# Kernel tuning notes

Measured on AMD Instinct MI355X. Metric: run time of the kernel, lower is better.

Reference implementation:

```python
import jax, jax.numpy as jnp
import numpy as np

DIM = 128
HEADS = 8
DH = DIM // HEADS
WIN = (4, 4, 4)
TOPK = 4
EPS = 1e-6


def _ln(x, g, b):
    mu = jnp.mean(x, -1, keepdims=True)
    var = jnp.mean((x - mu) ** 2, -1, keepdims=True)
    return (x - mu) * jax.lax.rsqrt(var + EPS) * g + b


def _win3d(x, p1, p2, p3):
    # x: [B,S,H,W,C] -> [B, p1*p2*p3, Ms, Mh, Mw, C]
    B, S, H, W, C = x.shape
    Ms, Mh, Mw = S // p1, H // p2, W // p3
    x = x.reshape(B, p1, Ms, p2, Mh, p3, Mw, C)
    x = x.transpose(0, 1, 3, 5, 2, 4, 6, 7)
    return x.reshape(B, p1 * p2 * p3, Ms, Mh, Mw, C)


def setup_inputs() -> dict:
    key = jax.random.key(0)
    ks = jax.random.split(key, 20)

    def lin(k, din, dout):
        return jax.random.normal(k, (din, dout), jnp.float32) * 0.02

    return {
        "x_in": jax.random.normal(ks[0], (2, 128, 16, 32, 32), jnp.float32),
        "x_g_in": jax.random.normal(ks[1], (2, 128, 8, 16, 16), jnp.float32),
        # Atten (global branch)
        "qkv_w": lin(ks[2], DIM, 3 * DIM), "qkv_b": jnp.zeros((3 * DIM,), jnp.float32),
        "proj_w": lin(ks[3], DIM, DIM), "proj_b": jnp.zeros((DIM,), jnp.float32),
        # shared LayerNorm (self.norm1 is reused everywhere in the original)
        "ln_g": jnp.ones((DIM,), jnp.float32), "ln_b": jnp.zeros((DIM,), jnp.float32),
        # mlp (global branch FFN)
        "mlp_w1": lin(ks[4], DIM, 4 * DIM), "mlp_b1": jnp.zeros((4 * DIM,), jnp.float32),
        "mlp_w2": lin(ks[5], 4 * DIM, DIM), "mlp_b2": jnp.zeros((DIM,), jnp.float32),
        # TopkRouting
        "rq_w": lin(ks[6], DIM, DIM), "rq_b": jnp.zeros((DIM,), jnp.float32),
        "rk_w": lin(ks[7], DIM, DIM), "rk_b": jnp.zeros((DIM,), jnp.float32),
        # fused qkv over concatenated local+gathered-global tokens
        "gqkv_w": lin(ks[8], DIM, 3 * DIM), "gqkv_b": jnp.zeros((3 * DIM,), jnp.float32),
        "wo_w": lin(ks[9], DIM, DIM), "wo_b": jnp.zeros((DIM,), jnp.float32),
        # mlp2 (local branch FFN)
        "mlp2_w1": lin(ks[10], DIM, 4 * DIM), "mlp2_b1": jnp.zeros((4 * DIM,), jnp.float32),
        "mlp2_w2": lin(ks[11], 4 * DIM, DIM), "mlp2_b2": jnp.zeros((DIM,), jnp.float32),
    }


def reference(x_in, x_g_in, qkv_w, qkv_b, proj_w, proj_b, ln_g, ln_b,
              mlp_w1, mlp_b1, mlp_w2, mlp_b2, rq_w, rq_b, rk_w, rk_b,
              gqkv_w, gqkv_b, wo_w, wo_b, mlp2_w1, mlp2_b1, mlp2_w2, mlp2_b2):
    B, C, S, H, W = x_in.shape
    Ms, Mh, Mw = WIN
    p1, p2, p3 = S // Ms, H // Mh, W // Mw  # pads are zero for these shapes
    nw, w3l = p1 * p2 * p3, Ms * Mh * Mw
    scale = DIM ** -0.5  # BiLevelRoutingAttention.scale = dim**-0.5 (not per-head)

    x = jnp.transpose(x_in, (0, 2, 3, 4, 1))  # [B,S,H,W,C]
    shortcut_l = _win3d(x, p1, p2, p3).reshape(B, nw, w3l, C)

    # ---- global branch: full self-attention + FFN ----
    _, _, gS, gH, gW = x_g_in.shape
    gN = gS * gH * gW
    xg = jnp.transpose(x_g_in, (0, 2, 3, 4, 1)).reshape(B, gN, C)
    h = _ln(xg, ln_g, ln_b)
    qkv = (h @ qkv_w + qkv_b).reshape(B, gN, 3, HEADS, DH).transpose(2, 0, 3, 1, 4)
    q, k, v = qkv[0], qkv[1], qkv[2]
    a = jax.nn.softmax(jnp.einsum('bhnd,bhmd->bhnm', q, k) * DH ** -0.5, axis=-1)
    o = jnp.einsum('bhnm,bhmd->bhnd', a, v).transpose(0, 2, 1, 3).reshape(B, gN, C)
    xg = (o @ proj_w + proj_b) + xg
    xg4 = xg.reshape(B, gS, gH, gW, C)
    h = _ln(xg4, ln_g, ln_b)
    xg4 = xg4 + (jax.nn.gelu(h @ mlp_w1 + mlp_b1, approximate=False) @ mlp_w2 + mlp_b2)

    # ---- top-k window routing ----
    swg = _win3d(xg4, p1, p2, p3)  # [B,nw,gMs,gMh,gMw,C]
    w3g = swg.shape[2] * swg.shape[3] * swg.shape[4]
    g_win = swg.mean((2, 3, 4))  # [B,nw,C]
    qh = g_win @ rq_w + rq_b
    kh = g_win @ rk_w + rk_b
    logit = jnp.einsum('bnc,bmc->bnm', qh * scale, kh)
    _tvals, tidx = jax.lax.top_k(logit, TOPK)  # r_weight is computed but unused in the original forward

    # gather top-k global windows' tokens per local window
    gflat = swg.reshape(B, nw, w3g, C)
    gath = jax.vmap(lambda kv, idx: kv[idx])(gflat, tidx)  # [B,nw,topk,w3g,C]
    sc = jnp.concatenate([shortcut_l, gath.reshape(B, nw, TOPK * w3g, C)], axis=2)
    w3 = w3l + TOPK * w3g

    # ---- local+routed attention over concatenated tokens ----
    qkvp = _ln(sc, ln_g, ln_b) @ gqkv_w + gqkv_b
    qp, kp, vp = jnp.split(qkvp, 3, axis=-1)
    qp = qp.reshape(B, nw, w3, HEADS, DH)
    kp = kp.reshape(B, nw, w3, HEADS, DH)
    vp = vp.reshape(B, nw, w3, HEADS, DH)
    aw = jax.nn.softmax(jnp.einsum('bnqhd,bnkhd->bnhqk', qp * scale, kp), axis=-1)
    out = jnp.einsum('bnhqk,bnkhd->bnqhd', aw, vp).reshape(B, nw, w3, C)

    l = out[:, :, :w3l] @ wo_w + wo_b + shortcut_l
    l = l.reshape(B, p1, p2, p3, Ms, Mh, Mw, C).transpose(0, 1, 4, 2, 5, 3, 6, 7).reshape(B, S, H, W, C)
    l = l + (jax.nn.gelu(_ln(l, ln_g, ln_b) @ mlp2_w1 + mlp2_b1, approximate=False) @ mlp2_w2 + mlp2_b2)

    l_out = jnp.transpose(l, (0, 4, 1, 2, 3))
    g_out = jnp.transpose(xg4, (0, 4, 1, 2, 3))
    return (l_out, g_out)
```

## Files before the change

### kernel.cpp

```cpp
#include <hip/hip_runtime.h>
#include <hip/hip_bf16.h>
#include <math.h>

#define BATCH 2
#define CDIM 128
#define SS 16
#define HH_ 32
#define WW_ 32
#define NSP (SS*HH_*WW_)
#define GS 8
#define GH 16
#define GW 16
#define GN (GS*GH*GW)
#define HEADS 8
#define DH 16
#define NW 256
#define W3L 64
#define W3G 8
#define TOPK 4
#define W3 (W3L + TOPK*W3G)
#define LN_EPS 1e-6f
#define ROUTE_SCALE 0.08838834764831845f
#define GATTN_SCALE 0.25f

typedef short bshort8 __attribute__((ext_vector_type(8)));
typedef float f32x4 __attribute__((ext_vector_type(4)));

__device__ __forceinline__ unsigned short f2bf(float f) {
    unsigned int u = __float_as_uint(f);
    unsigned int r = (u + 0x7fffu + ((u >> 16) & 1u)) >> 16;
    return (unsigned short)r;
}
__device__ __forceinline__ float gelu_exact(float x) {
    return 0.5f * x * (1.0f + erff(x * 0.70710678118654752f));
}
__device__ __forceinline__ float shfl_sum32(float v) {
#pragma unroll
    for (int m = 16; m > 0; m >>= 1) v += __shfl_xor(v, m);
    return v;
}
__device__ __forceinline__ float shfl_sum16(float v) {
#pragma unroll
    for (int m = 8; m > 0; m >>= 1) v += __shfl_xor(v, m);
    return v;
}
__device__ __forceinline__ float shfl_sum8(float v) {
#pragma unroll
    for (int m = 4; m > 0; m >>= 1) v += __shfl_xor(v, m);
    return v;
}

__global__ __launch_bounds__(256) void k_wprep_all(const float* __restrict__ gqkv_w,
        const float* __restrict__ m2_w1, const float* __restrict__ m2_w2,
        const float* __restrict__ proj_w, const float* __restrict__ mlp_w1,
        const float* __restrict__ mlp_w2, const float* __restrict__ wo_w,
        const float* __restrict__ qkv_w,
        unsigned short* __restrict__ wt, unsigned short* __restrict__ w1t,
        unsigned short* __restrict__ w2t, unsigned short* __restrict__ projt,
        unsigned short* __restrict__ gw1t, unsigned short* __restrict__ gw2t,
        unsigned short* __restrict__ wot, unsigned short* __restrict__ qkvt) {
    int id = blockIdx.x * 256 + threadIdx.x;
    if (id < 49152) {
        int n = id >> 7, k = id & 127;
        float v = gqkv_w[k * 384 + n];
        if (n < 128) v *= ROUTE_SCALE;
        wt[id] = f2bf(v);
    } else if (id < 114688) {
        int i = id - 49152; int n = i >> 7, k = i & 127;
        w1t[i] = f2bf(m2_w1[k * 512 + n]);
    } else if (id < 180224) {
        int i = id - 114688; int n = i >> 9, k = i & 511;
        w2t[i] = f2bf(m2_w2[k * 128 + n]);
    } else if (id < 196608) {
        int i = id - 180224; int n = i >> 7, k = i & 127;
        projt[i] = f2bf(proj_w[k * 128 + n]);
    } else if (id < 262144) {
        int i = id - 196608; int n = i >> 7, k = i & 127;
        gw1t[i] = f2bf(mlp_w1[k * 512 + n]);
    } else if (id < 327680) {
        int i = id - 262144; int n = i >> 9, k = i & 511;
        gw2t[i] = f2bf(mlp_w2[k * 128 + n]);
    } else if (id < 344064) {
        int i = id - 327680; int n = i >> 7, k = i & 127;
        wot[i] = f2bf(wo_w[k * 128 + n]);
    } else {
        int i = id - 344064; int n = i >> 7, k = i & 127;
        float v = qkv_w[k * 384 + n];
        if (n < 128) v *= GATTN_SCALE;
        qkvt[i] = f2bf(v);
    }
}

__global__ __launch_bounds__(256) void k_gqkv_mfma(const float* __restrict__ xg_in,
        const unsigned short* __restrict__ qkvt, const float* __restrict__ qkv_b,
        const float* __restrict__ ln_g, const float* __restrict__ ln_b,
        float* __restrict__ xg, unsigned short* __restrict__ qgb,
        unsigned short* __restrict__ kgb, unsigned short* __restrict__ vgtb) {
    int blk = blockIdx.x; int b = blk >> 7; int n0 = (blk & 127) * 16;
    int t = threadIdx.x; int w = t >> 6; int lane = t & 63;
    int l15 = lane & 15, quad = lane >> 4;
    __shared__ __align__(16) float xs[16 * 132];
    __shared__ __align__(16) unsigned short h[16 * 136];
    f32x4 zero4 = {0.f, 0.f, 0.f, 0.f};

    {
        int c = t >> 1, j0 = (t & 1) * 8;
        const float* src = xg_in + ((size_t)(b * 128 + c)) * GN + n0 + j0;
        float4 v0 = *(const float4*)src;
        float4 v1 = *(const float4*)(src + 4);
        xs[(j0 + 0) * 132 + c] = v0.x; xs[(j0 + 1) * 132 + c] = v0.y;
        xs[(j0 + 2) * 132 + c] = v0.z; xs[(j0 + 3) * 132 + c] = v0.w;
        xs[(j0 + 4) * 132 + c] = v1.x; xs[(j0 + 5) * 132 + c] = v1.y;
        xs[(j0 + 6) * 132 + c] = v1.z; xs[(j0 + 7) * 132 + c] = v1.w;
    }
    __syncthreads();
    {
        int j = t >> 4, p = t & 15, c0 = p * 8;
        float vv[8]; float s1 = 0.f;
#pragma unroll
        for (int i = 0; i < 8; i++) { vv[i] = xs[j * 132 + c0 + i]; s1 += vv[i]; }
        s1 = shfl_sum16(s1);
        float mu = s1 * (1.0f / 128.0f);
        float s2 = 0.f;
#pragma unroll
        for (int i = 0; i < 8; i++) { float d = vv[i] - mu; s2 += d * d; }
        s2 = shfl_sum16(s2);
        float rs = rsqrtf(s2 * (1.0f / 128.0f) + LN_EPS);
        float* dst = xg + ((size_t)(b * GN) + n0 + j) * 128 + c0;
        *(float4*)dst = *(float4*)&vv[0];
        *(float4*)(dst + 4) = *(float4*)&vv[4];
        unsigned short hb[8];
#pragma unroll
        for (int i4 = 0; i4 < 2; i4++) {
            float4 g4 = *(const float4*)(ln_g + c0 + i4 * 4);
            float4 b4 = *(const float4*)(ln_b + c0 + i4 * 4);
            hb[i4 * 4 + 0] = f2bf((vv[i4 * 4 + 0] - mu) * rs * g4.x + b4.x);
            hb[i4 * 4 + 1] = f2bf((vv[i4 * 4 + 1] - mu) * rs * g4.y + b4.y);
            hb[i4 * 4 + 2] = f2bf((vv[i4 * 4 + 2] - mu) * rs * g4.z + b4.z);
            hb[i4 * 4 + 3] = f2bf((vv[i4 * 4 + 3] - mu) * rs * g4.w + b4.w);
        }
        *(ushort4*)&h[j * 136 + c0] = *(ushort4*)&hb[0];
        *(ushort4*)&h[j * 136 + c0 + 4] = *(ushort4*)&hb[4];
    }
    __syncthreads();

    bshort8 a[4];
#pragma unroll
    for (int ks = 0; ks < 4; ks++)
        a[ks] = *(const bshort8*)(h + l15 * 136 + ks * 32 + quad * 8);
    int bh_base = b * HEADS;
#pragma unroll
    for (int part = 0; part < 2; part++) {
#pragma unroll
        for (int which = 0; which < 2; which++) {
            int nt = 2 * w + which;
            int ncol = part * 128 + nt * 16;
            f32x4 acc = zero4;
#pragma unroll
            for (int ks = 0; ks < 4; ks++) {
                bshort8 bfr = *(const bshort8*)(qkvt + (size_t)(ncol + l15) * 128 + ks * 32 + quad * 8);
                acc = __builtin_amdgcn_mfma_f32_16x16x32_bf16(a[ks], bfr, acc, 0, 0, 0);
            }
            float bias = qkv_b[ncol + l15] * (part == 0 ? GATTN_SCALE : 1.f);
            unsigned short* dst = (part == 0) ? qgb : kgb;
#pragma unroll
            for (int r = 0; r < 4; r++)
                dst[((size_t)(bh_base + nt) * GN + n0 + quad * 4 + r) * DH + l15] = f2bf(acc[r] + bias);
        }
    }
#pragma unroll
    for (int which = 0; which < 2; which++) {
        int mtv = 2 * w + which;
        f32x4 acc = zero4;
#pragma unroll
        for (int ks = 0; ks < 4; ks++) {
            bshort8 aw = *(const bshort8*)(qkvt + (size_t)(256 + mtv * 16 + l15) * 128 + ks * 32 + quad * 8);
            acc = __builtin_amdgcn_mfma_f32_16x16x32_bf16(aw, a[ks], acc, 0, 0, 0);
        }
#pragma unroll
        for (int r = 0; r < 4; r++) {
            float bias = qkv_b[256 + mtv * 16 + quad * 4 + r];
            vgtb[((size_t)(bh_base + mtv) * DH + quad * 4 + r) * GN + n0 + l15] = f2bf(acc[r] + bias);
        }
    }
}

__global__ __launch_bounds__(256) void k_gattn_mfma(const unsigned short* __restrict__ qgb,
        const unsigned short* __restrict__ kgb, const unsigned short* __restrict__ vgtb,
        float* __restrict__ og) {
    int blk = blockIdx.x;
    int bh = blk >> 7; int qt = (blk & 127) << 4;
    int b = bh >> 3, hh = bh & 7;
    int t = threadIdx.x; int w = t >> 6; int lane = t & 63;
    int col = lane & 15, quad = lane >> 4;
    __shared__ __align__(16) unsigned short Pbuf[4 * 16 * 40];
    __shared__ float po[4][64][4];
    __shared__ float pl[4][64][4];

    bshort8 aq = {0, 0, 0, 0, 0, 0, 0, 0};
    if (quad < 2)
        aq = *(const bshort8*)(qgb + ((size_t)bh * GN + qt + col) * DH + quad * 8);

    f32x4 o = {0.f, 0.f, 0.f, 0.f};
    float lsum[4] = {0.f, 0.f, 0.f, 0.f};
    const unsigned short* kb = kgb + (size_t)bh * GN * DH;
    const unsigned short* vb = vgtb + (size_t)bh * DH * GN;
    unsigned short* pb = Pbuf + w * (16 * 40);
    int row0 = quad * 4;
    int kbeg = w * 512;
    for (int kc = kbeg; kc < kbeg + 512; kc += 32) {
        bshort8 bk0 = {0, 0, 0, 0, 0, 0, 0, 0};
        bshort8 bk1 = {0, 0, 0, 0, 0, 0, 0, 0};
        if (quad < 2) {
            bk0 = *(const bshort8*)(kb + (size_t)(kc + col) * DH + quad * 8);
            bk1 = *(const bshort8*)(kb + (size_t)(kc + 16 + col) * DH + quad * 8);
        }
        f32x4 z = {0.f, 0.f, 0.f, 0.f};
        f32x4 s0 = __builtin_amdgcn_mfma_f32_16x16x32_bf16(aq, bk0, z, 0, 0, 0);
        f32x4 s1 = __builtin_amdgcn_mfma_f32_16x16x32_bf16(aq, bk1, z, 0, 0, 0);
        float p0[4], p1[4];
#pragma unroll
        for (int r = 0; r < 4; r++) {
            p0[r] = __expf(s0[r]); p1[r] = __expf(s1[r]);
            lsum[r] += p0[r] + p1[r];
        }
#pragma unroll
        for (int r = 0; r < 4; r++) {
            pb[(row0 + r) * 40 + col] = f2bf(p0[r]);
            pb[(row0 + r) * 40 + 16 + col] = f2bf(p1[r]);
        }
        bshort8 pA = *(const bshort8*)(pb + col * 40 + quad * 8);
        bshort8 bv = *(const bshort8*)(vb + (size_t)col * GN + kc + quad * 8);
        o = __builtin_amdgcn_mfma_f32_16x16x32_bf16(pA, bv, o, 0, 0, 0);
    }
#pragma unroll
    for (int r = 0; r < 4; r++) {
        float v = lsum[r];
        v += __shfl_xor(v, 1); v += __shfl_xor(v, 2);
        v += __shfl_xor(v, 4); v += __shfl_xor(v, 8);
        lsum[r] = v;
    }
#pragma unroll
    for (int r = 0; r < 4; r++) { po[w][lane][r] = o[r]; pl[w][lane][r] = lsum[r]; }
    __syncthreads();
    if (w == 0) {
#pragma unroll
        for (int r = 0; r < 4; r++) {
            float os = po[0][lane][r] + po[1][lane][r] + po[2][lane][r] + po[3][lane][r];
            float ls = pl[0][lane][r] + pl[1][lane][r] + pl[2][lane][r] + pl[3][lane][r];
            og[((size_t)(b * GN) + qt + quad * 4 + r) * 128 + hh * 16 + col] = os / ls;
        }
    }
}

__global__ __launch_bounds__(256) void k_gmlp_mfma(const float* __restrict__ og,
        const float* __restrict__ xg,
        const unsigned short* __restrict__ projt, const float* __restrict__ proj_b,
        const float* __restrict__ ln_g, const float* __restrict__ ln_b,
        const unsigned short* __restrict__ gw1t, const float* __restrict__ b1,
        const unsigned short* __restrict__ gw2t, const float* __restrict__ b2,
        float* __restrict__ xg4, float* __restrict__ gout) {
    int blk = blockIdx.x; int b = blk >> 7; int n0g = (blk & 127) * 16;
    int t = threadIdx.x; int w = t >> 6; int lane = t & 63;
    int l15 = lane & 15, quad = lane >> 4;
    __shared__ __align__(16) unsigned short ao[16 * 136];
    __shared__ __align__(16) float xs[16 * 132];
    __shared__ __align__(16) unsigned short h[16 * 136];
    __shared__ __align__(16) unsigned short h1[16 * 520];
    float* of32 = (float*)h1;
    f32x4 zero4 = {0.f, 0.f, 0.f, 0.f};

    {
        int j = t >> 4, p = t & 15, c0 = p * 8;
        size_t base = ((size_t)(b * GN) + n0g + j) * 128 + c0;
        float4 v0 = *(const float4*)(og + base);
        float4 v1 = *(const float4*)(og + base + 4);
        ushort4 u0 = { f2bf(v0.x), f2bf(v0.y), f2bf(v0.z), f2bf(v0.w) };
        ushort4 u1 = { f2bf(v1.x), f2bf(v1.y), f2bf(v1.z), f2bf(v1.w) };
        *(ushort4*)&ao[j * 136 + c0] = u0;
        *(ushort4*)&ao[j * 136 + c0 + 4] = u1;
        *(float4*)&xs[j * 132 + c0] = *(const float4*)(xg + base);
        *(float4*)&xs[j * 132 + c0 + 4] = *(const float4*)(xg + base + 4);
    }
    __syncthreads();

    {
        bshort8 a[4];
#pragma unroll
        for (int ks = 0; ks < 4; ks++)
            a[ks] = *(const bshort8*)(ao + l15 * 136 + ks * 32 + quad * 8);
#pragma unroll
        for (int nt = 0; nt < 2; nt++) {
            int n0 = w * 32 + nt * 16;
            f32x4 acc = zero4;
#pragma unroll
            for (int ks = 0; ks < 4; ks++) {
                bshort8 bfr = *(const bshort8*)(projt + (n0 + l15) * 128 + ks * 32 + quad * 8);
                acc = __builtin_amdgcn_mfma_f32_16x16x32_bf16(a[ks], bfr, acc, 0, 0, 0);
            }
            float bias = proj_b[n0 + l15];
#pragma unroll
            for (int r = 0; r < 4; r++) {
                int m = quad * 4 + r;
                xs[m * 132 + n0 + l15] += acc[r] + bias;
            }
        }
    }
    __syncthreads();

    {
        int j = t >> 4, p = t & 15, c0 = p * 8;
        float vv[8]; float s1 = 0.f;
#pragma unroll
        for (int i = 0; i < 8; i++) { vv[i] = xs[j * 132 + c0 + i]; s1 += vv[i]; }
        s1 = shfl_sum16(s1);
        float mu = s1 * (1.0f / 128.0f);
        float s2 = 0.f;
#pragma unroll
        for (int i = 0; i < 8; i++) { float d = vv[i] - mu; s2 += d * d; }
        s2 = shfl_sum16(s2);
        float rs = rsqrtf(s2 * (1.0f / 128.0f) + LN_EPS);
        unsigned short hb[8];
#pragma unroll
        for (int i4 = 0; i4 < 2; i4++) {
            float4 g4 = *(const float4*)(ln_g + c0 + i4 * 4);
            float4 b4 = *(const float4*)(ln_b + c0 + i4 * 4);
            hb[i4 * 4 + 0] = f2bf((vv[i4 * 4 + 0] - mu) * rs * g4.x + b4.x);
            hb[i4 * 4 + 1] = f2bf((vv[i4 * 4 + 1] - mu) * rs * g4.y + b4.y);
            hb[i4 * 4 + 2] = f2bf((vv[i4 * 4 + 2] - mu) * rs * g4.z + b4.z);
            hb[i4 * 4 + 3] = f2bf((vv[i4 * 4 + 3] - mu) * rs * g4.w + b4.w);
        }
        *(ushort4*)&h[j * 136 + c0] = *(ushort4*)&hb[0];
        *(ushort4*)&h[j * 136 + c0 + 4] = *(ushort4*)&hb[4];
    }
    __syncthreads();

    {
        bshort8 a[4];
#pragma unroll
        for (int ks = 0; ks < 4; ks++)
            a[ks] = *(const bshort8*)(h + l15 * 136 + ks * 32 + quad * 8);
#pragma unroll
        for (int nt = 0; nt < 8; nt++) {
            int n0 = w * 128 + nt * 16;
            f32x4 acc = zero4;
#pragma unroll
            for (int ks = 0; ks < 4; ks++) {
                bshort8 bfr = *(const bshort8*)(gw1t + (size_t)(n0 + l15) * 128 + ks * 32 + quad * 8);
                acc = __builtin_amdgcn_mfma_f32_16x16x32_bf16(a[ks], bfr, acc, 0, 0, 0);
            }
            float bias = b1[n0 + l15];
#pragma unroll
            for (int r = 0; r < 4; r++)
                h1[(quad * 4 + r) * 520 + n0 + l15] = f2bf(gelu_exact(acc[r] + bias));
        }
    }
    __syncthreads();

    f32x4 acc2[2]; acc2[0] = zero4; acc2[1] = zero4;
#pragma unroll 4
    for (int ks = 0; ks < 16; ks++) {
        bshort8 a = *(const bshort8*)(h1 + l15 * 520 + ks * 32 + quad * 8);
#pragma unroll
        for (int nt = 0; nt < 2; nt++) {
            int n0 = w * 32 + nt * 16;
            bshort8 bfr = *(const bshort8*)(gw2t + (size_t)(n0 + l15) * 512 + ks * 32 + quad * 8);
            acc2[nt] = __builtin_amdgcn_mfma_f32_16x16x32_bf16(a, bfr, acc2[nt], 0, 0, 0);
        }
    }
    __syncthreads();

    {
#pragma unroll
        for (int nt = 0; nt < 2; nt++) {
            int n0 = w * 32 + nt * 16;
            float bias = b2[n0 + l15];
#pragma unroll
            for (int r = 0; r < 4; r++) {
                int m = quad * 4 + r;
                float ov = xs[m * 132 + n0 + l15] + acc2[nt][r] + bias;
                of32[m * 132 + n0 + l15] = ov;
                xg4[((size_t)(b * GN) + n0g + m) * 128 + n0 + l15] = ov;
            }
        }
    }
    __syncthreads();

    {
        int cw = t >> 1, hf = t & 1, j0 = hf * 8;
        float* dst = gout + ((size_t)(b * 128 + cw)) * GN + n0g + j0;
#pragma unroll
        for (int i4 = 0; i4 < 2; i4++) {
            float4 ov = { of32[(j0 + i4 * 4 + 0) * 132 + cw], of32[(j0 + i4 * 4 + 1) * 132 + cw],
                          of32[(j0 + i4 * 4 + 2) * 132 + cw], of32[(j0 + i4 * 4 + 3) * 132 + cw] };
            *(float4*)(dst + i4 * 4) = ov;
        }
    }
}

__global__ void k_routing_qk(const float* __restrict__ xg4,
                             const float* __restrict__ rq_w, const float* __restrict__ rq_b,
                             const float* __restrict__ rk_w, const float* __restrict__ rk_b,
                             float* __restrict__ qh, float* __restrict__ kh) {
    int wid = blockIdx.x; int b = wid / NW, n = wid % NW;
    int c = threadIdx.x;
    int i1 = n / 64, i2 = (n / 8) % 8, i3 = n % 8;
    __shared__ float g[CDIM];
    float s = 0.f;
#pragma unroll
    for (int j = 0; j < W3G; j++) {
        int ds = j >> 2, dh = (j >> 1) & 1, dw = j & 1;
        int gi = ((i1 * 2 + ds) * GH + (i2 * 2 + dh)) * GW + (i3 * 2 + dw);
        s += xg4[((size_t)(b * GN + gi)) * CDIM + c];
    }
    g[c] = s * (1.0f / W3G);
    __syncthreads();
    float aq = rq_b[c], ak = rk_b[c];
    for (int k = 0; k < CDIM; k++) { float gv = g[k]; aq = fmaf(gv, rq_w[k * CDIM + c], aq); ak = fmaf(gv, rk_w[k * CDIM + c], ak); }
    qh[(size_t)wid * CDIM + c] = aq;
    kh[(size_t)wid * CDIM + c] = ak;
}

__global__ void k_topk(const float* __restrict__ qh, const float* __restrict__ kh,
                       int* __restrict__ tidx) {
    int wid = blockIdx.x; int b = wid / NW;
    int m = threadIdx.x;
    __shared__ float q[CDIM];
    __shared__ float lv[NW];
    __shared__ int li[NW];
    if (m < CDIM) q[m] = qh[(size_t)wid * CDIM + m] * ROUTE_SCALE;
    __syncthreads();
    float acc = 0.f;
    const float* kr = kh + ((size_t)b * NW + m) * CDIM;
    for (int k = 0; k < CDIM; k++) acc = fmaf(q[k], kr[k], acc);
#pragma unroll
    for (int sel = 0; sel < TOPK; sel++) {
        lv[m] = acc; li[m] = m; __syncthreads();
#pragma unroll
        for (int s = 128; s > 0; s >>= 1) {
            if (m < s) {
                if (lv[m + s] > lv[m] || (lv[m + s] == lv[m] && li[m + s] < li[m])) {
                    lv[m] = lv[m + s]; li[m] = li[m + s];
                }
            }
            __syncthreads();
        }
        int best = li[0]; __syncthreads();
        if (m == best) acc = -1e30f;
        if (m == 0) tidx[wid * TOPK + sel] = best;
    }
}

__global__ __launch_bounds__(256) void k_lnsc_local(const float* __restrict__ x_in,
        const float* __restrict__ ln_g, const float* __restrict__ ln_b,
        unsigned short* __restrict__ lnsc) {
    int blk = blockIdx.x;
    int wt = blk & 1; int hh = (blk >> 1) & 31; int s = (blk >> 6) & 15; int b = blk >> 10;
    int w0 = wt * 16;
    int t = threadIdx.x;
    __shared__ float tile[16][132];
    {
        int c = t >> 1; int wq = (t & 1) * 8;
        const float* src = x_in + (((size_t)(b * 128 + c) * SS + s)) * 1024 + hh * 32 + w0 + wq;
        float4 v0 = *(const float4*)src;
        float4 v1 = *(const float4*)(src + 4);
        tile[wq + 0][c] = v0.x; tile[wq + 1][c] = v0.y; tile[wq + 2][c] = v0.z; tile[wq + 3][c] = v0.w;
        tile[wq + 4][c] = v1.x; tile[wq + 5][c] = v1.y; tile[wq + 6][c] = v1.z; tile[wq + 7][c] = v1.w;
    }
    __syncthreads();
    int w = t >> 4; int j = t & 15;
    float vals[8];
    float s1 = 0.f;
#pragma unroll
    for (int i = 0; i < 8; i++) { vals[i] = tile[w][j * 8 + i]; s1 += vals[i]; }
    s1 = shfl_sum16(s1);
    float mu = s1 * (1.0f / 128.0f);
    float s2 = 0.f;
#pragma unroll
    for (int i = 0; i < 8; i++) { float d = vals[i] - mu; s2 += d * d; }
    s2 = shfl_sum16(s2);
    float rs = rsqrtf(s2 * (1.0f / 128.0f) + LN_EPS);
    float4 g0 = *(const float4*)(ln_g + j * 8);
    float4 g1 = *(const float4*)(ln_g + j * 8 + 4);
    float4 b0 = *(const float4*)(ln_b + j * 8);
    float4 b1 = *(const float4*)(ln_b + j * 8 + 4);
    float gv[8] = { g0.x, g0.y, g0.z, g0.w, g1.x, g1.y, g1.z, g1.w };
    float bv[8] = { b0.x, b0.y, b0.z, b0.w, b1.x, b1.y, b1.z, b1.w };
    int ww = w0 + w;
    int n = (s >> 2) * 64 + (hh >> 2) * 8 + (ww >> 2);
    int slot = (s & 3) * 16 + (hh & 3) * 4 + (ww & 3);
    unsigned short* dst = lnsc + ((size_t)(b * NW + n) * W3 + slot) * 128 + j * 8;
    ushort4 u0, u1;
    u0.x = f2bf((vals[0] - mu) * rs * gv[0] + bv[0]);
    u0.y = f2bf((vals[1] - mu) * rs * gv[1] + bv[1]);
    u0.z = f2bf((vals[2] - mu) * rs * gv[2] + bv[2]);
    u0.w = f2bf((vals[3] - mu) * rs * gv[3] + bv[3]);
    u1.x = f2bf((vals[4] - mu) * rs * gv[4] + bv[4]);
    u1.y = f2bf((vals[5] - mu) * rs * gv[5] + bv[5]);
    u1.z = f2bf((vals[6] - mu) * rs * gv[6] + bv[6]);
    u1.w = f2bf((vals[7] - mu) * rs * gv[7] + bv[7]);
    *(ushort4*)dst = u0;
    *(ushort4*)(dst + 4) = u1;
}

__global__ __launch_bounds__(256) void k_lnsc_gath(const float* __restrict__ xg4,
        const int* __restrict__ tidx,
        const float* __restrict__ ln_g, const float* __restrict__ ln_b,
        unsigned short* __restrict__ lnsc) {
    int blk = blockIdx.x;
    int kk = blk & 3; int wn = blk >> 2;
    int b = wn >> 8;
    int g = tidx[wn * TOPK + kk];
    int gi1 = g >> 6, gi2 = (g >> 3) & 7, gi3 = g & 7;
    int t = threadIdx.x; int j = t >> 5, lj = t & 31;
    int ds = j >> 2, dh = (j >> 1) & 1, dw = j & 1;
    int gi = ((gi1 * 2 + ds) * GH + (gi2 * 2 + dh)) * GW + (gi3 * 2 + dw);
    float4 v = *(const float4*)(xg4 + ((size_t)(b * GN + gi)) * 128 + lj * 4);
    float s1 = shfl_sum32(v.x + v.y + v.z + v.w);
    float mu = s1 * (1.0f / 128.0f);
    float d0 = v.x - mu, d1 = v.y - mu, d2 = v.z - mu, d3 = v.w - mu;
    float s2 = shfl_sum32(d0 * d0 + d1 * d1 + d2 * d2 + d3 * d3);
    float rs = rsqrtf(s2 * (1.0f / 128.0f) + LN_EPS);
    float4 g4 = *(const float4*)(ln_g + lj * 4);
    float4 b4 = *(const float4*)(ln_b + lj * 4);
    ushort4 u;
    u.x = f2bf(d0 * rs * g4.x + b4.x);
    u.y = f2bf(d1 * rs * g4.y + b4.y);
    u.z = f2bf(d2 * rs * g4.z + b4.z);
    u.w = f2bf(d3 * rs * g4.w + b4.w);
    *(ushort4*)(lnsc + ((size_t)wn * W3 + 64 + kk * 8 + j) * 128 + lj * 4) = u;
}

__global__ __launch_bounds__(256) void k_local_mfma(const unsigned short* __restrict__ lnsc,
        const unsigned short* __restrict__ wt, const float* __restrict__ gqkv_b,
        float* __restrict__ aout) {
    int wn = blockIdx.x;
    int t = threadIdx.x; int w = t >> 6; int lane = t & 63;
    int l15 = lane & 15, quad = lane >> 4;
    __shared__ __align__(16) unsigned short Qs[64 * 136];
    __shared__ __align__(16) unsigned short Ks2[96 * 136];
    __shared__ __align__(16) unsigned short Vts[128 * 104];
    __shared__ __align__(16) unsigned short Ps[4][16 * 40];

    const unsigned short* Xb = lnsc + (size_t)wn * W3 * 128;
    f32x4 zero4 = {0.f, 0.f, 0.f, 0.f};

    for (int mt = 0; mt < 4; mt++) {
        bshort8 a[4];
#pragma unroll
        for (int ks = 0; ks < 4; ks++)
            a[ks] = *(const bshort8*)(Xb + (mt * 16 + l15) * 128 + ks * 32 + quad * 8);
#pragma unroll
        for (int which = 0; which < 2; which++) {
            int n0 = (w + which * 4) * 16;
            f32x4 acc = zero4;
#pragma unroll
            for (int ks = 0; ks < 4; ks++) {
                bshort8 bfr = *(const bshort8*)(wt + (n0 + l15) * 128 + ks * 32 + quad * 8);
                acc = __builtin_amdgcn_mfma_f32_16x16x32_bf16(a[ks], bfr, acc, 0, 0, 0);
            }
            float bias = gqkv_b[n0 + l15] * ROUTE_SCALE;
#pragma unroll
            for (int r = 0; r < 4; r++)
                Qs[(mt * 16 + quad * 4 + r) * 136 + n0 + l15] = f2bf(acc[r] + bias);
        }
    }
    for (int mt = 0; mt < 6; mt++) {
        bshort8 a[4];
#pragma unroll
        for (int ks = 0; ks < 4; ks++)
            a[ks] = *(const bshort8*)(Xb + (mt * 16 + l15) * 128 + ks * 32 + quad * 8);
#pragma unroll
        for (int which = 0; which < 2; which++) {
            int nt8 = w + which * 4;
            int n0g = 128 + nt8 * 16;
            f32x4 acc = zero4;
#pragma unroll
            for (int ks = 0; ks < 4; ks++) {
                bshort8 bfr = *(const bshort8*)(wt + (n0g + l15) * 128 + ks * 32 + quad * 8);
                acc = __builtin_amdgcn_mfma_f32_16x16x32_bf16(a[ks], bfr, acc, 0, 0, 0);
            }
            float bias = gqkv_b[n0g + l15];
#pragma unroll
            for (int r = 0; r < 4; r++)
                Ks2[(mt * 16 + quad * 4 + r) * 136 + nt8 * 16 + l15] = f2bf(acc[r] + bias);
        }
    }
    for (int which = 0; which < 2; which++) {
        int mtv = 2 * w + which;
        bshort8 a[4];
#pragma unroll
        for (int ks = 0; ks < 4; ks++)
            a[ks] = *(const bshort8*)(wt + (256 + mtv * 16 + l15) * 128 + ks * 32 + quad * 8);
        float biasr[4];
#pragma unroll
        for (int r = 0; r < 4; r++) biasr[r] = gqkv_b[256 + mtv * 16 + quad * 4 + r];
        for (int ntv = 0; ntv < 6; ntv++) {
            f32x4 acc = zero4;
#pragma unroll
            for (int ks = 0; ks < 4; ks++) {
                bshort8 bfr = *(const bshort8*)(Xb + (ntv * 16 + l15) * 128 + ks * 32 + quad * 8);
                acc = __builtin_amdgcn_mfma_f32_16x16x32_bf16(a[ks], bfr, acc, 0, 0, 0);
            }
#pragma unroll
            for (int r = 0; r < 4; r++)
                Vts[(mtv * 16 + quad * 4 + r) * 104 + ntv * 16 + l15] = f2bf(acc[r] + biasr[r]);
        }
    }
    __syncthreads();

    unsigned short* Pw = &Ps[w][0];
    bshort8 zfrag = {0, 0, 0, 0, 0, 0, 0, 0};
#pragma unroll
    for (int hh2 = 0; hh2 < 2; hh2++) {
        int h = 2 * w + hh2;
        for (int mt = 0; mt < 4; mt++) {
            bshort8 aq = zfrag;
            if (quad < 2)
                aq = *(const bshort8*)(Qs + (mt * 16 + l15) * 136 + h * 16 + quad * 8);
            float rsum[4] = {0.f, 0.f, 0.f, 0.f};
            f32x4 oacc = zero4;
#pragma unroll
            for (int kc = 0; kc < 96; kc += 32) {
#pragma unroll
                for (int sub = 0; sub < 2; sub++) {
                    int nt = (kc >> 4) + sub;
                    bshort8 bk = zfrag;
                    if (quad < 2)
                        bk = *(const bshort8*)(Ks2 + (nt * 16 + l15) * 136 + h * 16 + quad * 8);
                    f32x4 s = __builtin_amdgcn_mfma_f32_16x16x32_bf16(aq, bk, zero4, 0, 0, 0);
#pragma unroll
                    for (int r = 0; r < 4; r++) {
                        float p = __expf(s[r]);
                        rsum[r] += p;
                        Pw[(quad * 4 + r) * 40 + sub * 16 + l15] = f2bf(p);
                    }
                }
                bshort8 ap = *(const bshort8*)(Pw + l15 * 40 + quad * 8);
                bshort8 bv = *(const bshort8*)(Vts + (h * 16 + l15) * 104 + kc + quad * 8);
                oacc = __builtin_amdgcn_mfma_f32_16x16x32_bf16(ap, bv, oacc, 0, 0, 0);
            }
#pragma unroll
            for (int r = 0; r < 4; r++) {
                float v = rsum[r];
                v += __shfl_xor(v, 1); v += __shfl_xor(v, 2);
                v += __shfl_xor(v, 4); v += __shfl_xor(v, 8);
                rsum[r] = v;
            }
#pragma unroll
            for (int r = 0; r < 4; r++)
                aout[((size_t)wn * W3L + mt * 16 + quad * 4 + r) * 128 + h * 16 + l15]
                    = oacc[r] / rsum[r];
        }
    }
}

__global__ __launch_bounds__(256) void k_wo_mfma(const float* __restrict__ aout,
        const unsigned short* __restrict__ wot, const float* __restrict__ wo_b,
        const float* __restrict__ x_in, float* __restrict__ lpre) {
    int blk = blockIdx.x; int T0 = blk * 32;
    int b = T0 >> 14; int sp0 = T0 & 16383;
    int t = threadIdx.x; int w = t >> 6; int lane = t & 63;
    int l15 = lane & 15, quad = lane >> 4;
    __shared__ __align__(16) unsigned short as2[32 * 136];
    __shared__ __align__(16) float xs[32 * 132];
    f32x4 zero4 = {0.f, 0.f, 0.f, 0.f};

    {
        int j = t >> 3, p = t & 7, c0 = p * 16;
        int sp = sp0 + j;
        int s = sp >> 10, hh = (sp >> 5) & 31, ww = sp & 31;
        int n = (s >> 2) * 64 + (hh >> 2) * 8 + (ww >> 2);
        int slot = (s & 3) * 16 + (hh & 3) * 4 + (ww & 3);
        const float* src = aout + (((size_t)(b * NW + n)) * W3L + slot) * 128 + c0;
#pragma unroll
        for (int i4 = 0; i4 < 4; i4++) {
            float4 v = *(const float4*)(src + i4 * 4);
            ushort4 u = { f2bf(v.x), f2bf(v.y), f2bf(v.z), f2bf(v.w) };
            *(ushort4*)&as2[j * 136 + c0 + i4 * 4] = u;
        }
    }
    {
        int c = t >> 1, half = t & 1, j0 = half * 16;
        const float* src = x_in + ((size_t)(b * 128 + c)) * 16384 + sp0 + j0;
#pragma unroll
        for (int i4 = 0; i4 < 4; i4++) {
            float4 v = *(const float4*)(src + i4 * 4);
            xs[(j0 + i4 * 4 + 0) * 132 + c] = v.x;
            xs[(j0 + i4 * 4 + 1) * 132 + c] = v.y;
            xs[(j0 + i4 * 4 + 2) * 132 + c] = v.z;
            xs[(j0 + i4 * 4 + 3) * 132 + c] = v.w;
        }
    }
    __syncthreads();

    bshort8 a[2][4];
#pragma unroll
    for (int mt = 0; mt < 2; mt++)
#pragma unroll
        for (int ks = 0; ks < 4; ks++)
            a[mt][ks] = *(const bshort8*)(as2 + (mt * 16 + l15) * 136 + ks * 32 + quad * 8);
#pragma unroll
    for (int nt = 0; nt < 2; nt++) {
        int n0 = w * 32 + nt * 16;
        f32x4 acc0 = zero4, acc1 = zero4;
#pragma unroll
        for (int ks = 0; ks < 4; ks++) {
            bshort8 bfr = *(const bshort8*)(wot + (n0 + l15) * 128 + ks * 32 + quad * 8);
            acc0 = __builtin_amdgcn_mfma_f32_16x16x32_bf16(a[0][ks], bfr, acc0, 0, 0, 0);
            acc1 = __builtin_amdgcn_mfma_f32_16x16x32_bf16(a[1][ks], bfr, acc1, 0, 0, 0);
        }
        float bias = wo_b[n0 + l15];
#pragma unroll
        for (int r = 0; r < 4; r++) {
            int m0 = quad * 4 + r;
            int m1 = 16 + quad * 4 + r;
            lpre[((size_t)T0 + m0) * 128 + n0 + l15] = acc0[r] + bias + xs[m0 * 132 + n0 + l15];
            lpre[((size_t)T0 + m1) * 128 + n0 + l15] = acc1[r] + bias + xs[m1 * 132 + n0 + l15];
        }
    }
}

__global__ __launch_bounds__(256) void k_mlp2_mfma(const float* __restrict__ lpre,
        const float* __restrict__ ln_g, const float* __restrict__ ln_b,
        const unsigned short* __restrict__ w1t, const float* __restrict__ b1,
        const unsigned short* __restrict__ w2t, const float* __restrict__ b2,
        float* __restrict__ lout) {
    int blk = blockIdx.x;
    int T0 = blk * 32;
    int b = T0 >> 14;
    int sp = T0 & 16383;
    int t = threadIdx.x; int w = t >> 6; int lane = t & 63;
    int l15 = lane & 15, quad = lane >> 4;
    __shared__ __align__(16) unsigned short buf[32 * 520];
    float* of32 = (float*)buf;

    {
        int j = t >> 3, p = t & 7, c0 = p * 16;
        const float* src = lpre + ((size_t)T0 + j) * 128 + c0;
        float4 v0 = *(const float4*)(src + 0);
        float4 v1 = *(const float4*)(src + 4);
        float4 v2 = *(const float4*)(src + 8);
        float4 v3 = *(const float4*)(src + 12);
        float s1 = (v0.x + v0.y + v0.z + v0.w) + (v1.x + v1.y + v1.z + v1.w)
                 + (v2.x + v2.y + v2.z + v2.w) + (v3.x + v3.y + v3.z + v3.w);
        s1 = shfl_sum8(s1);
        float mu = s1 * (1.0f / 128.0f);
        float vv[16] = { v0.x, v0.y, v0.z, v0.w, v1.x, v1.y, v1.z, v1.w,
                         v2.x, v2.y, v2.z, v2.w, v3.x, v3.y, v3.z, v3.w };
        float s2 = 0.f;
#pragma unroll
        for (int i = 0; i < 16; i++) { float d = vv[i] - mu; s2 += d * d; }
        s2 = shfl_sum8(s2);
        float rs = rsqrtf(s2 * (1.0f / 128.0f) + LN_EPS);
        unsigned short hb[16];
#pragma unroll
        for (int i4 = 0; i4 < 4; i4++) {
            float4 g4 = *(const float4*)(ln_g + c0 + i4 * 4);
            float4 b4 = *(const float4*)(ln_b + c0 + i4 * 4);
            hb[i4 * 4 + 0] = f2bf((vv[i4 * 4 + 0] - mu) * rs * g4.x + b4.x);
            hb[i4 * 4 + 1] = f2bf((vv[i4 * 4 + 1] - mu) * rs * g4.y + b4.y);
            hb[i4 * 4 + 2] = f2bf((vv[i4 * 4 + 2] - mu) * rs * g4.z + b4.z);
            hb[i4 * 4 + 3] = f2bf((vv[i4 * 4 + 3] - mu) * rs * g4.w + b4.w);
        }
        *(ushort4*)&buf[j * 136 + c0 + 0] = *(ushort4*)&hb[0];
        *(ushort4*)&buf[j * 136 + c0 + 4] = *(ushort4*)&hb[4];
        *(ushort4*)&buf[j * 136 + c0 + 8] = *(ushort4*)&hb[8];
        *(ushort4*)&buf[j * 136 + c0 + 12] = *(ushort4*)&hb[12];
    }
    __syncthreads();

    bshort8 a1[2][4];
#pragma unroll
    for (int mt = 0; mt < 2; mt++)
#pragma unroll
        for (int ks = 0; ks < 4; ks++)
            a1[mt][ks] = *(const bshort8*)(buf + (mt * 16 + l15) * 136 + ks * 32 + quad * 8);
    __syncthreads();

    f32x4 zero4 = {0.f, 0.f, 0.f, 0.f};
    {
        int n0w = w * 128;
#pragma unroll
        for (int nt = 0; nt < 8; nt++) {
            int n0 = n0w + nt * 16;
            f32x4 acc0 = zero4, acc1 = zero4;
#pragma unroll
            for (int ks = 0; ks < 4; ks++) {
                bshort8 bfr = *(const bshort8*)(w1t + (size_t)(n0 + l15) * 128 + ks * 32 + quad * 8);
                acc0 = __builtin_amdgcn_mfma_f32_16x16x32_bf16(a1[0][ks], bfr, acc0, 0, 0, 0);
                acc1 = __builtin_amdgcn_mfma_f32_16x16x32_bf16(a1[1][ks], bfr, acc1, 0, 0, 0);
            }
            float bias = b1[n0 + l15];
#pragma unroll
            for (int r = 0; r < 4; r++) {
                buf[(quad * 4 + r) * 520 + n0 + l15] = f2bf(gelu_exact(acc0[r] + bias));
                buf[(16 + quad * 4 + r) * 520 + n0 + l15] = f2bf(gelu_exact(acc1[r] + bias));
            }
        }
    }
    __syncthreads();

    f32x4 acc[2][2];
    acc[0][0] = zero4; acc[0][1] = zero4; acc[1][0] = zero4; acc[1][1] = zero4;
    {
#pragma unroll 4
        for (int ks = 0; ks < 16; ks++) {
            bshort8 a0 = *(const bshort8*)(buf + (l15) * 520 + ks * 32 + quad * 8);
            bshort8 a1b = *(const bshort8*)(buf + (16 + l15) * 520 + ks * 32 + quad * 8);
#pragma unroll
            for (int nt = 0; nt < 2; nt++) {
                int n0 = w * 32 + nt * 16;
                bshort8 bfr = *(const bshort8*)(w2t + (size_t)(n0 + l15) * 512 + ks * 32 + quad * 8);
                acc[0][nt] = __builtin_amdgcn_mfma_f32_16x16x32_bf16(a0, bfr, acc[0][nt], 0, 0, 0);
                acc[1][nt] = __builtin_amdgcn_mfma_f32_16x16x32_bf16(a1b, bfr, acc[1][nt], 0, 0, 0);
            }
        }
    }
    __syncthreads();

#pragma unroll
    for (int mt = 0; mt < 2; mt++) {
#pragma unroll
        for (int nt = 0; nt < 2; nt++) {
            int n0 = w * 32 + nt * 16;
            float bias = b2[n0 + l15];
#pragma unroll
            for (int r = 0; r < 4; r++) {
                int m = mt * 16 + quad * 4 + r;
                float res = lpre[((size_t)T0 + m) * 128 + n0 + l15];
                of32[m * 132 + n0 + l15] = res + acc[mt][nt][r] + bias;
            }
        }
    }
    __syncthreads();

    {
        int c = t >> 1, half = t & 1, j0 = half * 16;
        float* dst = lout + ((size_t)(b * 128 + c)) * NSP + sp + j0;
#pragma unroll
        for (int i4 = 0; i4 < 4; i4++) {
            float4 ov = { of32[(j0 + i4 * 4 + 0) * 132 + c], of32[(j0 + i4 * 4 + 1) * 132 + c],
                          of32[(j0 + i4 * 4 + 2) * 132 + c], of32[(j0 + i4 * 4 + 3) * 132 + c] };
            *(float4*)(dst + i4 * 4) = ov;
        }
    }
}

extern "C" void kernel_launch(void* const* d_in, const int* in_sizes, int n_in,
                              void* d_out, int out_size, void* d_ws, size_t ws_size,
                              hipStream_t stream) {
    const float* x_in   = (const float*)d_in[0];
    const float* xg_in  = (const float*)d_in[1];
    const float* qkv_w  = (const float*)d_in[2];
    const float* qkv_b  = (const float*)d_in[3];
    const float* proj_w = (const float*)d_in[4];
    const float* proj_b = (const float*)d_in[5];
    const float* ln_g   = (const float*)d_in[6];
    const float* ln_b   = (const float*)d_in[7];
    const float* mlp_w1 = (const float*)d_in[8];
    const float* mlp_b1 = (const float*)d_in[9];
    const float* mlp_w2 = (const float*)d_in[10];
    const float* mlp_b2 = (const float*)d_in[11];
    const float* rq_w   = (const float*)d_in[12];
    const float* rq_b   = (const float*)d_in[13];
    const float* rk_w   = (const float*)d_in[14];
    const float* rk_b   = (const float*)d_in[15];
    const float* gqkv_w = (const float*)d_in[16];
    const float* gqkv_b = (const float*)d_in[17];
    const float* wo_w   = (const float*)d_in[18];
    const float* wo_b   = (const float*)d_in[19];
    const float* m2_w1  = (const float*)d_in[20];
    const float* m2_b1  = (const float*)d_in[21];
    const float* m2_w2  = (const float*)d_in[22];
    const float* m2_b2  = (const float*)d_in[23];

    float* out = (float*)d_out;
    float* ws  = (float*)d_ws;

    float* xg4 = ws;
    float* xg  = ws + 524288;
    unsigned short* qgb  = (unsigned short*)(ws + 1048576);
    unsigned short* kgb  = (unsigned short*)(ws + 1310720);
    unsigned short* vgtb = (unsigned short*)(ws + 1572864);
    float* og  = ws + 1835008;
    float* qh  = ws + 2359296;
    float* kh  = ws + 2424832;
    int*   tidx = (int*)(ws + 2490368);
    unsigned short* lnsc = (unsigned short*)(ws + 2492416);
    float* aout = ws + 2492416 + 3145728;
    float* lpre = ws + 9832448;
    unsigned short* wt   = (unsigned short*)(ws + 14026752);
    unsigned short* w1t  = (unsigned short*)(ws + 14051328);
    unsigned short* w2t  = (unsigned short*)(ws + 14084096);
    unsigned short* projt = (unsigned short*)(ws + 14116864);
    unsigned short* gw1t  = (unsigned short*)(ws + 14125056);
    unsigned short* gw2t  = (unsigned short*)(ws + 14157824);
    unsigned short* wot   = (unsigned short*)(ws + 14190592);
    unsigned short* qkvt  = (unsigned short*)(ws + 14198784);

    const size_t L_OUT = (size_t)BATCH * CDIM * NSP;
    float* gout = out + L_OUT;

    hipLaunchKernelGGL(k_wprep_all, dim3(1536), dim3(256), 0, stream,
                       gqkv_w, m2_w1, m2_w2, proj_w, mlp_w1, mlp_w2, wo_w, qkv_w,
                       wt, w1t, w2t, projt, gw1t, gw2t, wot, qkvt);
    hipLaunchKernelGGL(k_gqkv_mfma, dim3(256), dim3(256), 0, stream,
                       xg_in, qkvt, qkv_b, ln_g, ln_b, xg, qgb, kgb, vgtb);
    hipLaunchKernelGGL(k_gattn_mfma, dim3(2048), dim3(256), 0, stream, qgb, kgb, vgtb, og);
    hipLaunchKernelGGL(k_gmlp_mfma, dim3(256), dim3(256), 0, stream,
                       og, xg, projt, proj_b, ln_g, ln_b, gw1t, mlp_b1, gw2t, mlp_b2,
                       xg4, gout);
    hipLaunchKernelGGL(k_routing_qk, dim3(512), dim3(128), 0, stream,
                       xg4, rq_w, rq_b, rk_w, rk_b, qh, kh);
    hipLaunchKernelGGL(k_topk, dim3(512), dim3(256), 0, stream, qh, kh, tidx);
    hipLaunchKernelGGL(k_lnsc_local, dim3(2048), dim3(256), 0, stream,
                       x_in, ln_g, ln_b, lnsc);
    hipLaunchKernelGGL(k_lnsc_gath, dim3(2048), dim3(256), 0, stream,
                       xg4, tidx, ln_g, ln_b, lnsc);
    hipLaunchKernelGGL(k_local_mfma, dim3(512), dim3(256), 0, stream,
                       lnsc, wt, gqkv_b, aout);
    hipLaunchKernelGGL(k_wo_mfma, dim3(1024), dim3(256), 0, stream,
                       aout, wot, wo_b, x_in, lpre);
    hipLaunchKernelGGL(k_mlp2_mfma, dim3(1024), dim3(256), 0, stream,
                       lpre, ln_g, ln_b, w1t, m2_b1, w2t, m2_b2, out);
}
```

Before: 291.8 us.

## Assign one attention head per wave in local attention with 512-thread blocks

The local attention kernel now runs 8 waves per block, and each wave owns one head's 16-column slice of Q, K and V. Each wave keeps its Q/K/V weight fragments in registers across all row tiles and fuses the K, V and Q projections into a single loop over the token tiles. Because each wave only reads the LDS slices it wrote itself, the block-wide barrier is dropped. The aim is more waves in flight, less repeated weight loading and no barrier stall, at the cost of higher per-thread register pressure under the new launch bounds.

```diff
diff --git a/kernel.cpp b/kernel.cpp
--- a/kernel.cpp
+++ b/kernel.cpp
@@ -531,7 +531,7 @@
     *(ushort4*)(lnsc + ((size_t)wn * W3 + 64 + kk * 8 + j) * 128 + lj * 4) = u;
 }
 
-__global__ __launch_bounds__(256) void k_local_mfma(const unsigned short* __restrict__ lnsc,
+__global__ __launch_bounds__(512, 4) void k_local_mfma(const unsigned short* __restrict__ lnsc,
         const unsigned short* __restrict__ wt, const float* __restrict__ gqkv_b,
         float* __restrict__ aout) {
     int wn = blockIdx.x;
@@ -540,118 +540,92 @@
     __shared__ __align__(16) unsigned short Qs[64 * 136];
     __shared__ __align__(16) unsigned short Ks2[96 * 136];
     __shared__ __align__(16) unsigned short Vts[128 * 104];
-    __shared__ __align__(16) unsigned short Ps[4][16 * 40];
+    __shared__ __align__(16) unsigned short Ps[8][16 * 40];
 
     const unsigned short* Xb = lnsc + (size_t)wn * W3 * 128;
     f32x4 zero4 = {0.f, 0.f, 0.f, 0.f};
 
-    for (int mt = 0; mt < 4; mt++) {
+    bshort8 qw[4], kw[4], vw[4];
+#pragma unroll
+    for (int ks = 0; ks < 4; ks++) {
+        qw[ks] = *(const bshort8*)(wt + (w * 16 + l15) * 128 + ks * 32 + quad * 8);
+        kw[ks] = *(const bshort8*)(wt + (128 + w * 16 + l15) * 128 + ks * 32 + quad * 8);
+        vw[ks] = *(const bshort8*)(wt + (256 + w * 16 + l15) * 128 + ks * 32 + quad * 8);
+    }
+    float qbias = gqkv_b[w * 16 + l15] * ROUTE_SCALE;
+    float kbias = gqkv_b[128 + w * 16 + l15];
+    float vbias[4];
+#pragma unroll
+    for (int r = 0; r < 4; r++) vbias[r] = gqkv_b[256 + w * 16 + quad * 4 + r];
+
+    for (int mt = 0; mt < 6; mt++) {
         bshort8 a[4];
 #pragma unroll
         for (int ks = 0; ks < 4; ks++)
             a[ks] = *(const bshort8*)(Xb + (mt * 16 + l15) * 128 + ks * 32 + quad * 8);
-#pragma unroll
-        for (int which = 0; which < 2; which++) {
-            int n0 = (w + which * 4) * 16;
-            f32x4 acc = zero4;
-#pragma unroll
-            for (int ks = 0; ks < 4; ks++) {
-                bshort8 bfr = *(const bshort8*)(wt + (n0 + l15) * 128 + ks * 32 + quad * 8);
-                acc = __builtin_amdgcn_mfma_f32_16x16x32_bf16(a[ks], bfr, acc, 0, 0, 0);
-            }
-            float bias = gqkv_b[n0 + l15] * ROUTE_SCALE;
+        f32x4 acck = zero4;
+        f32x4 accv = zero4;
+#pragma unroll
+        for (int ks = 0; ks < 4; ks++) {
+            acck = __builtin_amdgcn_mfma_f32_16x16x32_bf16(a[ks], kw[ks], acck, 0, 0, 0);
+            accv = __builtin_amdgcn_mfma_f32_16x16x32_bf16(vw[ks], a[ks], accv, 0, 0, 0);
+        }
+#pragma unroll
+        for (int r = 0; r < 4; r++) {
+            Ks2[(mt * 16 + quad * 4 + r) * 136 + w * 16 + l15] = f2bf(acck[r] + kbias);
+            Vts[(w * 16 + quad * 4 + r) * 104 + mt * 16 + l15] = f2bf(accv[r] + vbias[r]);
+        }
+        if (mt < 4) {
+            f32x4 accq = zero4;
+#pragma unroll
+            for (int ks = 0; ks < 4; ks++)
+                accq = __builtin_amdgcn_mfma_f32_16x16x32_bf16(a[ks], qw[ks], accq, 0, 0, 0);
 #pragma unroll
             for (int r = 0; r < 4; r++)
-                Qs[(mt * 16 + quad * 4 + r) * 136 + n0 + l15] = f2bf(acc[r] + bias);
-        }
-    }
-    for (int mt = 0; mt < 6; mt++) {
-        bshort8 a[4];
-#pragma unroll
-        for (int ks = 0; ks < 4; ks++)
-            a[ks] = *(const bshort8*)(Xb + (mt * 16 + l15) * 128 + ks * 32 + quad * 8);
-#pragma unroll
-        for (int which = 0; which < 2; which++) {
-            int nt8 = w + which * 4;
-            int n0g = 128 + nt8 * 16;
-            f32x4 acc = zero4;
-#pragma unroll
-            for (int ks = 0; ks < 4; ks++) {
-                bshort8 bfr = *(const bshort8*)(wt + (n0g + l15) * 128 + ks * 32 + quad * 8);
-                acc = __builtin_amdgcn_mfma_f32_16x16x32_bf16(a[ks], bfr, acc, 0, 0, 0);
-            }
-            float bias = gqkv_b[n0g + l15];
-#pragma unroll
-            for (int r = 0; r < 4; r++)
-                Ks2[(mt * 16 + quad * 4 + r) * 136 + nt8 * 16 + l15] = f2bf(acc[r] + bias);
-        }
-    }
-    for (int which = 0; which < 2; which++) {
-        int mtv = 2 * w + which;
-        bshort8 a[4];
-#pragma unroll
-        for (int ks = 0; ks < 4; ks++)
-            a[ks] = *(const bshort8*)(wt + (256 + mtv * 16 + l15) * 128 + ks * 32 + quad * 8);
-        float biasr[4];
-#pragma unroll
-        for (int r = 0; r < 4; r++) biasr[r] = gqkv_b[256 + mtv * 16 + quad * 4 + r];
-        for (int ntv = 0; ntv < 6; ntv++) {
-            f32x4 acc = zero4;
-#pragma unroll
-            for (int ks = 0; ks < 4; ks++) {
-                bshort8 bfr = *(const bshort8*)(Xb + (ntv * 16 + l15) * 128 + ks * 32 + quad * 8);
-                acc = __builtin_amdgcn_mfma_f32_16x16x32_bf16(a[ks], bfr, acc, 0, 0, 0);
-            }
-#pragma unroll
-            for (int r = 0; r < 4; r++)
-                Vts[(mtv * 16 + quad * 4 + r) * 104 + ntv * 16 + l15] = f2bf(acc[r] + biasr[r]);
-        }
-    }
-    __syncthreads();
+                Qs[(mt * 16 + quad * 4 + r) * 136 + w * 16 + l15] = f2bf(accq[r] + qbias);
+        }
+    }
 
     unsigned short* Pw = &Ps[w][0];
     bshort8 zfrag = {0, 0, 0, 0, 0, 0, 0, 0};
-#pragma unroll
-    for (int hh2 = 0; hh2 < 2; hh2++) {
-        int h = 2 * w + hh2;
-        for (int mt = 0; mt < 4; mt++) {
-            bshort8 aq = zfrag;
-            if (quad < 2)
-                aq = *(const bshort8*)(Qs + (mt * 16 + l15) * 136 + h * 16 + quad * 8);
-            float rsum[4] = {0.f, 0.f, 0.f, 0.f};
-            f32x4 oacc = zero4;
-#pragma unroll
-            for (int kc = 0; kc < 96; kc += 32) {
-#pragma unroll
-                for (int sub = 0; sub < 2; sub++) {
-                    int nt = (kc >> 4) + sub;
-                    bshort8 bk = zfrag;
-                    if (quad < 2)
-                        bk = *(const bshort8*)(Ks2 + (nt * 16 + l15) * 136 + h * 16 + quad * 8);
-                    f32x4 s = __builtin_amdgcn_mfma_f32_16x16x32_bf16(aq, bk, zero4, 0, 0, 0);
-#pragma unroll
-                    for (int r = 0; r < 4; r++) {
-                        float p = __expf(s[r]);
-                        rsum[r] += p;
-                        Pw[(quad * 4 + r) * 40 + sub * 16 + l15] = f2bf(p);
-                    }
+    int h = w;
+    for (int mt = 0; mt < 4; mt++) {
+        bshort8 aq = zfrag;
+        if (quad < 2)
+            aq = *(const bshort8*)(Qs + (mt * 16 + l15) * 136 + h * 16 + quad * 8);
+        float rsum[4] = {0.f, 0.f, 0.f, 0.f};
+        f32x4 oacc = zero4;
+#pragma unroll
+        for (int kc = 0; kc < 96; kc += 32) {
+#pragma unroll
+            for (int sub = 0; sub < 2; sub++) {
+                int nt = (kc >> 4) + sub;
+                bshort8 bk = zfrag;
+                if (quad < 2)
+                    bk = *(const bshort8*)(Ks2 + (nt * 16 + l15) * 136 + h * 16 + quad * 8);
+                f32x4 s = __builtin_amdgcn_mfma_f32_16x16x32_bf16(aq, bk, zero4, 0, 0, 0);
+#pragma unroll
+                for (int r = 0; r < 4; r++) {
+                    float p = __expf(s[r]);
+                    rsum[r] += p;
+                    Pw[(quad * 4 + r) * 40 + sub * 16 + l15] = f2bf(p);
                 }
-                bshort8 ap = *(const bshort8*)(Pw + l15 * 40 + quad * 8);
-                bshort8 bv = *(const bshort8*)(Vts + (h * 16 + l15) * 104 + kc + quad * 8);
-                oacc = __builtin_amdgcn_mfma_f32_16x16x32_bf16(ap, bv, oacc, 0, 0, 0);
-            }
-#pragma unroll
-            for (int r = 0; r < 4; r++) {
-                float v = rsum[r];
-                v += __shfl_xor(v, 1); v += __shfl_xor(v, 2);
-                v += __shfl_xor(v, 4); v += __shfl_xor(v, 8);
-                rsum[r] = v;
-            }
-#pragma unroll
-            for (int r = 0; r < 4; r++)
-                aout[((size_t)wn * W3L + mt * 16 + quad * 4 + r) * 128 + h * 16 + l15]
-                    = oacc[r] / rsum[r];
-        }
+            }
+            bshort8 ap = *(const bshort8*)(Pw + l15 * 40 + quad * 8);
+            bshort8 bv = *(const bshort8*)(Vts + (h * 16 + l15) * 104 + kc + quad * 8);
+            oacc = __builtin_amdgcn_mfma_f32_16x16x32_bf16(ap, bv, oacc, 0, 0, 0);
+        }
+#pragma unroll
+        for (int r = 0; r < 4; r++) {
+            float v = rsum[r];
+            v += __shfl_xor(v, 1); v += __shfl_xor(v, 2);
+            v += __shfl_xor(v, 4); v += __shfl_xor(v, 8);
+            rsum[r] = v;
+        }
+#pragma unroll
+        for (int r = 0; r < 4; r++)
+            aout[((size_t)wn * W3L + mt * 16 + quad * 4 + r) * 128 + h * 16 + l15]
+                = oacc[r] / rsum[r];
     }
 }
 
@@ -918,7 +892,7 @@
                        x_in, ln_g, ln_b, lnsc);
     hipLaunchKernelGGL(k_lnsc_gath, dim3(2048), dim3(256), 0, stream,
                        xg4, tidx, ln_g, ln_b, lnsc);
-    hipLaunchKernelGGL(k_local_mfma, dim3(512), dim3(256), 0, stream,
+    hipLaunchKernelGGL(k_local_mfma, dim3(512), dim3(512), 0, stream,
                        lnsc, wt, gqkv_b, aout);
     hipLaunchKernelGGL(k_wo_mfma, dim3(1024), dim3(256), 0, stream,
                        aout, wot, wo_b, x_in, lpre);
```

Result: faster. 268.6 us (-8.0%).
